# Optimization experiments

Hardware: AMD Instinct MI355X
Metric: run time of the kernel (lower is better)

The kernel has to match this reference:

```python
import jax, jax.numpy as jnp
import numpy as np

KERNEL_EPSILON = 0.001


def setup_inputs() -> dict:
    key = jax.random.key(0)
    k1, k2, k3 = jax.random.split(key, 3)
    B, H, S, D = 4, 16, 4096, 64
    return {
        "query": jax.random.normal(k1, (B, H, S, D), dtype=jnp.float32),
        "key": jax.random.normal(k2, (B, H, S, D), dtype=jnp.float32),
        "value": jax.random.normal(k3, (B, H, S, D), dtype=jnp.float32),
        "mask": jnp.ones((B, S), dtype=jnp.float32),
    }


def reference(query, key, value, mask):
    # ReLU feature map + epsilon
    q = jax.nn.relu(query) + KERNEL_EPSILON          # [B,H,S,D]
    k = jax.nn.relu(key) + KERNEL_EPSILON            # [B,H,S,D]
    k = k * mask[:, None, :, None]                   # mask keys
    # kv: [B,H,D,E] = sum_s k[...,s,d] * v[...,s,e]  (done first: linear attention)
    kv = jnp.einsum("bhsd,bhse->bhde", k, value)
    numerator = jnp.einsum("bhsd,bhde->bhse", q, kv)  # [B,H,S,D]
    k_sum = jnp.sum(k, axis=-2)                       # [B,H,D]
    denominator = jnp.einsum("bhsd,bhd->bhs", q, k_sum)[..., None]
    return numerator / denominator
```

## Files before the change

kernel.cpp:

```cpp
#include <hip/hip_runtime.h>


namespace {
constexpr int kB = 4, kH = 16, kS = 4096, kD = 64;
constexpr int kBH = kB * kH;
constexpr float kEps = 0.001f;

constexpr int KVSZ = kD * kD;
constexpr int SEG  = KVSZ + kD;
constexpr int F4PS = SEG / 4;
}

__global__ __launch_bounds__(256, 2)
void pa_kv_partial(const float* __restrict__ key, const float* __restrict__ value,
                   const float* __restrict__ mask, float* __restrict__ P, int ch1) {
  __shared__ float smem[4096];

  const int tid  = threadIdx.x;
  const int wid  = tid >> 6;
  const int lane = tid & 63;

  const int bh    = blockIdx.x / ch1;
  const int chunk = blockIdx.x - bh * ch1;
  const int b     = bh >> 4;
  const int rows  = kS / ch1;
  const int s0    = chunk * rows;
  const int tiles = rows >> 5;

  const float* kb = key   + (size_t)bh * kS * kD;
  const float* vb = value + (size_t)bh * kS * kD;
  const float* mb = mask  + (size_t)b * kS;

  float* ksT = smem + wid * 1024;
  float* vsT = smem + wid * 1024 + 512;

  const int lrow = lane >> 4;
  const int lcol = (lane & 15) << 2;
  const int ti   = lane >> 3;
  const int tj   = lane & 7;

  float acc[8][8];
#pragma unroll
  for (int i = 0; i < 8; ++i)
#pragma unroll
    for (int j = 0; j < 8; ++j) acc[i][j] = 0.f;
  float4 ksacc = make_float4(0.f, 0.f, 0.f, 0.f);

  int ts = s0 + wid * 8;
  float4 kq0 = *(const float4*)(kb + (size_t)(ts + lrow) * kD + lcol);
  float4 kq1 = *(const float4*)(kb + (size_t)(ts + 4 + lrow) * kD + lcol);
  float4 vq0 = *(const float4*)(vb + (size_t)(ts + lrow) * kD + lcol);
  float4 vq1 = *(const float4*)(vb + (size_t)(ts + 4 + lrow) * kD + lcol);
  float  m0  = mb[ts + lrow];
  float  m1  = mb[ts + 4 + lrow];

  for (int t = 0; t < tiles; ++t) {
    float4 kt0, kt1;
    kt0.x = (fmaxf(kq0.x, 0.f) + kEps) * m0;
    kt0.y = (fmaxf(kq0.y, 0.f) + kEps) * m0;
    kt0.z = (fmaxf(kq0.z, 0.f) + kEps) * m0;
    kt0.w = (fmaxf(kq0.w, 0.f) + kEps) * m0;
    kt1.x = (fmaxf(kq1.x, 0.f) + kEps) * m1;
    kt1.y = (fmaxf(kq1.y, 0.f) + kEps) * m1;
    kt1.z = (fmaxf(kq1.z, 0.f) + kEps) * m1;
    kt1.w = (fmaxf(kq1.w, 0.f) + kEps) * m1;

    ksacc.x += kt0.x + kt1.x;
    ksacc.y += kt0.y + kt1.y;
    ksacc.z += kt0.z + kt1.z;
    ksacc.w += kt0.w + kt1.w;

    *(float4*)&ksT[lrow * 64 + lcol]       = kt0;
    *(float4*)&ksT[(lrow + 4) * 64 + lcol] = kt1;
    *(float4*)&vsT[lrow * 64 + lcol]       = vq0;
    *(float4*)&vsT[(lrow + 4) * 64 + lcol] = vq1;

    if (t + 1 < tiles) {
      ts += 32;
      kq0 = *(const float4*)(kb + (size_t)(ts + lrow) * kD + lcol);
      kq1 = *(const float4*)(kb + (size_t)(ts + 4 + lrow) * kD + lcol);
      vq0 = *(const float4*)(vb + (size_t)(ts + lrow) * kD + lcol);
      vq1 = *(const float4*)(vb + (size_t)(ts + 4 + lrow) * kD + lcol);
      m0  = mb[ts + lrow];
      m1  = mb[ts + 4 + lrow];
    }

#pragma unroll
    for (int ss = 0; ss < 8; ++ss) {
      const float4 kf0 = *(const float4*)&ksT[ss * 64 + 8 * ti];
      const float4 kf1 = *(const float4*)&ksT[ss * 64 + 8 * ti + 4];
      const float4 vf0 = *(const float4*)&vsT[ss * 64 + 8 * tj];
      const float4 vf1 = *(const float4*)&vsT[ss * 64 + 8 * tj + 4];
      const float ka[8] = {kf0.x, kf0.y, kf0.z, kf0.w, kf1.x, kf1.y, kf1.z, kf1.w};
      const float va[8] = {vf0.x, vf0.y, vf0.z, vf0.w, vf1.x, vf1.y, vf1.z, vf1.w};
#pragma unroll
      for (int i = 0; i < 8; ++i)
#pragma unroll
        for (int j = 0; j < 8; ++j) acc[i][j] = fmaf(ka[i], va[j], acc[i][j]);
    }
  }

  float* Pd = P + (size_t)(blockIdx.x * 4 + wid) * SEG;
#pragma unroll
  for (int i = 0; i < 8; ++i)
#pragma unroll
    for (int jj = 0; jj < 2; ++jj) {
      const int j = i * 2 + jj;
      const float4 o = make_float4(acc[i][jj * 4 + 0], acc[i][jj * 4 + 1],
                                   acc[i][jj * 4 + 2], acc[i][jj * 4 + 3]);
      *(float4*)&Pd[(size_t)(j * 64 + lane) * 4] = o;
    }

  ksacc.x += __shfl_xor(ksacc.x, 16); ksacc.x += __shfl_xor(ksacc.x, 32);
  ksacc.y += __shfl_xor(ksacc.y, 16); ksacc.y += __shfl_xor(ksacc.y, 32);
  ksacc.z += __shfl_xor(ksacc.z, 16); ksacc.z += __shfl_xor(ksacc.z, 32);
  ksacc.w += __shfl_xor(ksacc.w, 16); ksacc.w += __shfl_xor(ksacc.w, 32);
  if (lane < 16) *(float4*)&Pd[KVSZ + 4 * lane] = ksacc;
}

__global__ __launch_bounds__(256)
void pa_reduce(const float* __restrict__ P, float* __restrict__ R, int nseg) {
  const int gid = blockIdx.x * 256 + threadIdx.x;
  if (gid >= kBH * F4PS) return;
  const int bh  = gid / F4PS;
  const int pos = gid - bh * F4PS;

  const float* base = P + (size_t)bh * nseg * SEG + (size_t)pos * 4;
  float ax = 0.f, ay = 0.f, az = 0.f, aw = 0.f;
  for (int c = 0; c < nseg; ++c) {
    const float4 t = *(const float4*)(base + (size_t)c * SEG);
    ax += t.x; ay += t.y; az += t.z; aw += t.w;
  }

  int dpos;
  if (pos < KVSZ / 4) {
    const int j  = pos >> 6, ln = pos & 63;
    const int d  = 8 * (ln >> 3) + (j >> 1);
    const int e4 = 2 * (ln & 7) + (j & 1);
    dpos = d * 16 + e4;
  } else {
    dpos = pos;
  }
  *(float4*)&R[(size_t)bh * SEG + (size_t)dpos * 4] = make_float4(ax, ay, az, aw);
}

__global__ __launch_bounds__(256)
void pa_out(const float* __restrict__ query, const float* __restrict__ R,
            float* __restrict__ out) {
  __shared__ float ost[64 * 68];

  const int tid    = threadIdx.x;
  const int bh     = blockIdx.x >> 4;
  const int rowblk = blockIdx.x & 15;
  const int s      = rowblk * 256 + tid;

  const float* qrow = query + ((size_t)bh * kS + s) * kD;
  const float* Rb   = R + (size_t)bh * SEG;

  float4 acc[16];
#pragma unroll
  for (int e = 0; e < 16; ++e) acc[e] = make_float4(0.f, 0.f, 0.f, 0.f);
  float den = 0.f;

#pragma unroll 4
  for (int d4 = 0; d4 < 16; ++d4) {
    const float4 qv = *(const float4*)(qrow + 4 * d4);
    const float qd[4] = {fmaxf(qv.x, 0.f) + kEps, fmaxf(qv.y, 0.f) + kEps,
                         fmaxf(qv.z, 0.f) + kEps, fmaxf(qv.w, 0.f) + kEps};
#pragma unroll
    for (int dd = 0; dd < 4; ++dd) {
      const int d = 4 * d4 + dd;
      den = fmaf(qd[dd], Rb[KVSZ + d], den);
      const float* kvr = Rb + d * 64;
#pragma unroll
      for (int e = 0; e < 16; ++e) {
        acc[e].x = fmaf(qd[dd], kvr[4 * e + 0], acc[e].x);
        acc[e].y = fmaf(qd[dd], kvr[4 * e + 1], acc[e].y);
        acc[e].z = fmaf(qd[dd], kvr[4 * e + 2], acc[e].z);
        acc[e].w = fmaf(qd[dd], kvr[4 * e + 3], acc[e].w);
      }
    }
  }

  const float inv = 1.0f / den;
#pragma unroll
  for (int e = 0; e < 16; ++e) {
    acc[e].x *= inv; acc[e].y *= inv; acc[e].z *= inv; acc[e].w *= inv;
  }

  float* ob = out + ((size_t)bh * kS + (size_t)rowblk * 256) * kD;
  const int wid = tid >> 6, l = tid & 63;
  for (int bb = 0; bb < 4; ++bb) {
    if (wid == bb) {
#pragma unroll
      for (int e = 0; e < 16; ++e) *(float4*)&ost[l * 68 + 4 * e] = acc[e];
    }
    __syncthreads();
#pragma unroll
    for (int jj = 0; jj < 4; ++jj) {
      const int g = tid + 256 * jj;
      const int r = g >> 4, c = g & 15;
      *(float4*)&ob[(size_t)(bb * 64 + r) * kD + 4 * c] =
          *(const float4*)&ost[r * 68 + 4 * c];
    }
    __syncthreads();
  }
}

extern "C" void kernel_launch(void* const* d_in, const int* in_sizes, int n_in,
                              void* d_out, int out_size, void* d_ws, size_t ws_size,
                              hipStream_t stream) {
  const float* query = (const float*)d_in[0];
  const float* key   = (const float*)d_in[1];
  const float* value = (const float*)d_in[2];
  const float* mask  = (const float*)d_in[3];
  float* outp = (float*)d_out;

  auto need = [](int ch1) -> size_t {
    return (size_t)(kBH * 4 * ch1 + kBH) * SEG * sizeof(float);
  };
  int CH1 = 2;
  if (ws_size >= need(8)) CH1 = 8;
  else if (ws_size >= need(4)) CH1 = 4;

  float* P = (float*)d_ws;
  float* R = P + (size_t)kBH * 4 * CH1 * SEG;

  hipLaunchKernelGGL(pa_kv_partial, dim3(kBH * CH1), dim3(256), 0, stream,
                     key, value, mask, P, CH1);
  hipLaunchKernelGGL(pa_reduce, dim3((kBH * F4PS + 255) / 256), dim3(256), 0, stream,
                     P, R, 4 * CH1);
  hipLaunchKernelGGL(pa_out, dim3(kBH * 16), dim3(256), 0, stream,
                     query, R, outp);
}
```

Measured before the change: 255.7 us.

## Reduce per-wave kv partials in shared memory before writing block partial

Each block now sums its four waves' 64x64 kv partials and k-sums in shared memory, using serialized accumulation with barriers, and writes one segment per block instead of four. This cuts partial-buffer global writes and the reduce kernel's read volume by a factor of four. The chunk count rises to 16 when the workspace allows, and the occupancy hint is raised to 4 blocks per CU. The trade-off is extra barriers and serialized shared-memory passes at the end of each block, plus register pressure from the tighter launch bound.

```diff
diff --git a/kernel.cpp b/kernel.cpp
--- a/kernel.cpp
+++ b/kernel.cpp
@@ -11,10 +11,11 @@
 constexpr int F4PS = SEG / 4;
 }
 
-__global__ __launch_bounds__(256, 2)
+__global__ __launch_bounds__(256, 4)
 void pa_kv_partial(const float* __restrict__ key, const float* __restrict__ value,
                    const float* __restrict__ mask, float* __restrict__ P, int ch1) {
   __shared__ float smem[4096];
+  __shared__ float ksm[256];
 
   const int tid  = threadIdx.x;
   const int wid  = tid >> 6;
@@ -100,22 +101,42 @@
     }
   }
 
-  float* Pd = P + (size_t)(blockIdx.x * 4 + wid) * SEG;
-#pragma unroll
-  for (int i = 0; i < 8; ++i)
-#pragma unroll
-    for (int jj = 0; jj < 2; ++jj) {
-      const int j = i * 2 + jj;
-      const float4 o = make_float4(acc[i][jj * 4 + 0], acc[i][jj * 4 + 1],
-                                   acc[i][jj * 4 + 2], acc[i][jj * 4 + 3]);
-      *(float4*)&Pd[(size_t)(j * 64 + lane) * 4] = o;
-    }
-
   ksacc.x += __shfl_xor(ksacc.x, 16); ksacc.x += __shfl_xor(ksacc.x, 32);
   ksacc.y += __shfl_xor(ksacc.y, 16); ksacc.y += __shfl_xor(ksacc.y, 32);
   ksacc.z += __shfl_xor(ksacc.z, 16); ksacc.z += __shfl_xor(ksacc.z, 32);
   ksacc.w += __shfl_xor(ksacc.w, 16); ksacc.w += __shfl_xor(ksacc.w, 32);
-  if (lane < 16) *(float4*)&Pd[KVSZ + 4 * lane] = ksacc;
+  if (lane < 16) *(float4*)&ksm[wid * 64 + 4 * lane] = ksacc;
+
+#pragma unroll
+  for (int w = 0; w < 4; ++w) {
+    __syncthreads();
+    if (wid == w) {
+#pragma unroll
+      for (int i = 0; i < 8; ++i)
+#pragma unroll
+        for (int jj = 0; jj < 2; ++jj) {
+          const int j = i * 2 + jj;
+          float4 o = make_float4(acc[i][jj * 4 + 0], acc[i][jj * 4 + 1],
+                                 acc[i][jj * 4 + 2], acc[i][jj * 4 + 3]);
+          float* p = &smem[(size_t)(j * 64 + lane) * 4];
+          if (w != 0) {
+            const float4 prev = *(const float4*)p;
+            o.x += prev.x; o.y += prev.y; o.z += prev.z; o.w += prev.w;
+          }
+          *(float4*)p = o;
+        }
+    }
+  }
+  __syncthreads();
+
+  float* Pd = P + (size_t)blockIdx.x * SEG;
+#pragma unroll
+  for (int i = 0; i < 4; ++i) {
+    const int idx = tid + 256 * i;
+    *(float4*)&Pd[(size_t)idx * 4] = *(const float4*)&smem[(size_t)idx * 4];
+  }
+  if (tid < kD)
+    Pd[KVSZ + tid] = ksm[tid] + ksm[64 + tid] + ksm[128 + tid] + ksm[192 + tid];
 }
 
 __global__ __launch_bounds__(256)
@@ -217,19 +238,18 @@
   float* outp = (float*)d_out;
 
   auto need = [](int ch1) -> size_t {
-    return (size_t)(kBH * 4 * ch1 + kBH) * SEG * sizeof(float);
+    return (size_t)(kBH * ch1 + kBH) * SEG * sizeof(float);
   };
-  int CH1 = 2;
-  if (ws_size >= need(8)) CH1 = 8;
-  else if (ws_size >= need(4)) CH1 = 4;
+  int CH1 = 8;
+  if (ws_size >= need(16)) CH1 = 16;
 
   float* P = (float*)d_ws;
-  float* R = P + (size_t)kBH * 4 * CH1 * SEG;
+  float* R = P + (size_t)kBH * CH1 * SEG;
 
   hipLaunchKernelGGL(pa_kv_partial, dim3(kBH * CH1), dim3(256), 0, stream,
                      key, value, mask, P, CH1);
   hipLaunchKernelGGL(pa_reduce, dim3((kBH * F4PS + 255) / 256), dim3(256), 0, stream,
-                     P, R, 4 * CH1);
+                     P, R, CH1);
   hipLaunchKernelGGL(pa_out, dim3(kBH * 16), dim3(256), 0, stream,
                      query, R, outp);
 }
```

Result: slower. 430.2 us (+68.3%).
